# Kernel optimization log

Hardware: AMD Instinct MI355X
Metric: run time of the kernel (lower is better)

## Reference

```python
import jax, jax.numpy as jnp
import numpy as np

B = 8
C_IN = 3
IMG = 64
NF = 32
N_CALLS = 8
LAT = 512
KSIZES = [2 ** i + 1 for i in range(1, int(np.log2(IMG) - 1))]  # [3, 5, 9, 17]
N_SCALES = len(KSIZES)
C_FACTOR = 3 * N_SCALES          # identity + sobel-x + sobel-y per scale
GROUPS = C_FACTOR // 3           # 4
F = NF * C_FACTOR                # 384 expanded channels
CG = F // GROUPS                 # 96 channels per group
DK_TOT = 3 * GROUPS * CG * CG + 3 * F   # 111744 dynamic weights+biases
DK_HID = 2 * LAT                 # lat_factor = 2
OUT_CH = NF + NF + NF + 1        # 97 (multi_cut split sizes)
STATE = NF + NF * IMG + NF * IMG + IMG * IMG  # 8224


def _leaky(x):
    return jax.nn.leaky_relu(x, 0.2)


def _sobel_pair(k):
    c = jnp.linspace(-1.0, 1.0, k)
    gx = jnp.cos(0.5 * jnp.pi * c)[:, None] * jnp.sin(0.5 * jnp.pi * c)[None, :]
    return gx, gx.T


def sin_sobel(x):
    # fixed multi-scale depthwise sin-sobel filters, mode='split_out':
    # per scale concat [x, gx(x) all chans, gy(x) all chans]
    Bx, C, H, W = x.shape
    outs = []
    for k in KSIZES:
        gx, gy = _sobel_pair(k)
        w = jnp.broadcast_to(jnp.stack([gx, gy])[None], (C, 2, k, k)).reshape(C * 2, 1, k, k)
        p = (k - 1) // 2
        y = jax.lax.conv_general_dilated(x, w.astype(x.dtype), (1, 1), [(p, p), (p, p)],
                                         feature_group_count=C,
                                         dimension_numbers=('NCHW', 'OIHW', 'NCHW'))
        y = y.reshape(Bx, C, 2, H, W).transpose(0, 2, 1, 3, 4).reshape(Bx, 2 * C, H, W)
        outs.append(jnp.concatenate([x, y], axis=1))
    return jnp.concatenate(outs, axis=1)  # [B, 3*C*n_scales, H, W]


def instance_norm(x, eps=1e-5):
    m = x.mean(axis=(2, 3), keepdims=True)
    v = ((x - m) ** 2).mean(axis=(2, 3), keepdims=True)
    return (x - m) * jax.lax.rsqrt(v + eps)


def lin_res(x, Ws, bs, W0, b0, W1, b1):
    # LinearResidualBlock: shortcut + 0.1 * MLP
    return x @ Ws + bs + 0.1 * (_leaky(x @ W0 + b0) @ W1 + b1)


def conv1x1(x, w, b):
    return jnp.einsum('oi,bihw->bohw', w, x) + b[None, :, None, None]


def res_block(x, c0w, c0b, c1w, c1b, csw, csb):
    # ResidualBlock (1x1 convs): conv_s(x) + 0.1 * conv1(lrelu(conv0(lrelu(x))))
    dx = conv1x1(_leaky(x), c0w, c0b)
    dx = conv1x1(_leaky(dx), c1w, c1b)
    return conv1x1(x, csw, csb) + 0.1 * dx


def dyna_res_block(x, lat, Ws, bs, W0, b0, W1, b1):
    # DynaResidualBlock: per-sample grouped 1x1 conv weights generated from lat
    Bx, Fc, H, W = x.shape
    ks = lin_res(lat, Ws, bs, W0, b0, W1, b1)  # [B, DK_TOT]
    S = GROUPS * CG * CG
    k_in, k_mid, k_out, b_in, b_mid, b_out = jnp.split(
        ks, [S, 2 * S, 3 * S, 3 * S + Fc, 3 * S + 2 * Fc], axis=1)
    k_in = k_in.reshape(Bx, GROUPS, CG, CG)
    k_mid = k_mid.reshape(Bx, GROUPS, CG, CG)
    k_out = k_out.reshape(Bx, GROUPS, CG, CG)
    xg = x.reshape(Bx, GROUPS, CG, H, W)
    h = jnp.einsum('bgoi,bgihw->bgohw', k_in, xg) + b_in.reshape(Bx, GROUPS, CG, 1, 1)
    h = _leaky(h)
    h = jnp.einsum('bgoi,bgihw->bgohw', k_mid, h) + b_mid.reshape(Bx, GROUPS, CG, 1, 1)
    h = _leaky(h)
    h = jnp.einsum('bgoi,bgihw->bgohw', k_out, h) + b_out.reshape(Bx, GROUPS, CG, 1, 1)
    return x + h.reshape(Bx, Fc, H, W)  # identity shortcut (fin == fout)


def _forward(x, inj_lat, in_conv_w, in_conv_b, fl_Ws, fl_bs, fl_W0, fl_b0, fl_W1, fl_b1,
             dk_Ws, dk_bs, dk_W0, dk_b0, dk_W1, dk_b1,
             fc_c0w, fc_c0b, fc_c1w, fc_c1b, fc_csw, fc_csb,
             out_conv_w, out_conv_b, otl_w, otl_b):
    Bs = x.shape[0]
    out = conv1x1(x, in_conv_w, in_conv_b)
    out_embs = [out]
    lat = inj_lat
    for c in range(N_CALLS):
        lat = lat + 0.1 * lin_res(lat, fl_Ws[c], fl_bs[c], fl_W0[c], fl_b0[c], fl_W1[c], fl_b1[c])
        z = sin_sobel(out)
        z = instance_norm(z)
        z = z * jax.nn.sigmoid(dyna_res_block(z, lat, dk_Ws, dk_bs, dk_W0, dk_b0, dk_W1, dk_b1))
        z = res_block(z, fc_c0w, fc_c0b, fc_c1w, fc_c1b, fc_csw, fc_csb)
        out = out + 0.1 * z
        out_embs.append(out)
    # NOTE: source applies frac_conv(out) again here, but frac_conv expects
    # n_filter*c_factor (384) input channels while out has n_filter (32);
    # that line would raise in torch, so it is omitted (see notes).
    y = conv1x1(out, out_conv_w, out_conv_b)  # [B, 97, H, W]
    f, fh, fw, hw = jnp.split(y, [NF, 2 * NF, 3 * NF], axis=1)
    state = jnp.concatenate([
        f.mean(axis=(2, 3)),
        fh.mean(axis=3).reshape(Bs, -1),
        fw.mean(axis=2).reshape(Bs, -1),
        hw.reshape(Bs, -1),
    ], axis=1)  # [B, STATE]
    lat_out = state @ otl_w + otl_b
    return lat_out, jnp.stack(out_embs)


def setup_inputs():
    key = jax.random.key(0)
    ks = jax.random.split(key, 16)
    s = 0.02
    return {
        'x': jax.random.normal(ks[0], (B, C_IN, IMG, IMG), jnp.float32),
        'inj_lat': jax.random.normal(ks[1], (B, LAT), jnp.float32),
        'in_conv_w': jax.random.normal(ks[2], (NF, C_IN), jnp.float32) * s,
        'in_conv_b': jnp.zeros((NF,), jnp.float32),
        'fl_Ws': jax.random.normal(ks[3], (N_CALLS, LAT, LAT), jnp.float32) * s,
        'fl_bs': jnp.zeros((N_CALLS, LAT), jnp.float32),
        'fl_W0': jax.random.normal(ks[4], (N_CALLS, LAT, LAT), jnp.float32) * s,
        'fl_b0': jnp.zeros((N_CALLS, LAT), jnp.float32),
        'fl_W1': jax.random.normal(ks[5], (N_CALLS, LAT, LAT), jnp.float32) * s,
        'fl_b1': jnp.zeros((N_CALLS, LAT), jnp.float32),
        'dk_Ws': jax.random.normal(ks[6], (LAT, DK_TOT), jnp.float32) * s,
        'dk_bs': jnp.zeros((DK_TOT,), jnp.float32),
        'dk_W0': jax.random.normal(ks[7], (LAT, DK_HID), jnp.float32) * s,
        'dk_b0': jnp.zeros((DK_HID,), jnp.float32),
        'dk_W1': jax.random.normal(ks[8], (DK_HID, DK_TOT), jnp.float32) * s,
        'dk_b1': jnp.zeros((DK_TOT,), jnp.float32),
        'fc_c0w': jax.random.normal(ks[9], (F, F), jnp.float32) * s,
        'fc_c0b': jnp.zeros((F,), jnp.float32),
        'fc_c1w': jax.random.normal(ks[10], (NF, F), jnp.float32) * s,
        'fc_c1b': jnp.zeros((NF,), jnp.float32),
        'fc_csw': jax.random.normal(ks[11], (NF, F), jnp.float32) * s,
        'fc_csb': jnp.zeros((NF,), jnp.float32),
        'out_conv_w': jax.random.normal(ks[12], (OUT_CH, NF), jnp.float32) * s,
        'out_conv_b': jnp.zeros((OUT_CH,), jnp.float32),
        'otl_w': jax.random.normal(ks[13], (STATE, LAT), jnp.float32) * s,
        'otl_b': jnp.zeros((LAT,), jnp.float32),
    }


def reference(x, inj_lat, in_conv_w, in_conv_b, fl_Ws, fl_bs, fl_W0, fl_b0, fl_W1, fl_b1,
              dk_Ws, dk_bs, dk_W0, dk_b0, dk_W1, dk_b1,
              fc_c0w, fc_c0b, fc_c1w, fc_c1b, fc_csw, fc_csb,
              out_conv_w, out_conv_b, otl_w, otl_b):
    return _forward(x, inj_lat, in_conv_w, in_conv_b, fl_Ws, fl_bs, fl_W0, fl_b0, fl_W1, fl_b1,
                    dk_Ws, dk_bs, dk_W0, dk_b0, dk_W1, dk_b1,
                    fc_c0w, fc_c0b, fc_c1w, fc_c1b, fc_csw, fc_csb,
                    out_conv_w, out_conv_b, otl_w, otl_b)
```

## Files before the change

kernel.cpp:

```cpp
#include <hip/hip_runtime.h>

#define DEV __device__ __forceinline__

typedef __attribute__((ext_vector_type(4))) float  f32x4;
typedef __attribute__((ext_vector_type(8))) short  s16x8;
typedef __attribute__((ext_vector_type(4))) short  s16x4;

union FragU { s16x8 v; unsigned short h[8]; };
union U4    { s16x4 v; unsigned short h[4]; };

DEV float lrelu(float x){ return x > 0.f ? x : 0.2f*x; }
DEV unsigned short bfrne(float f){
    unsigned u = __builtin_bit_cast(unsigned, f);
    u += 0x7fffu + ((u>>16)&1u);
    return (unsigned short)(u>>16);
}
DEV float bf2f(unsigned short h){
    unsigned u = ((unsigned)h)<<16; return __builtin_bit_cast(float,u);
}
DEV f32x4 mfma16(s16x8 a, s16x8 b, f32x4 c){
    return __builtin_amdgcn_mfma_f32_16x16x32_bf16(a, b, c, 0, 0, 0);
}
DEV float wave_sum(float v){
    #pragma unroll
    for(int m=32;m>0;m>>=1) v += __shfl_xor(v, m, 64);
    return v;
}
DEV void blk_reduce2(float& a, float& b, float* sm){
    a = wave_sum(a); b = wave_sum(b);
    int wv = threadIdx.x>>6, ln = threadIdx.x&63;
    if(ln==0){ sm[wv*2]=a; sm[wv*2+1]=b; }
    __syncthreads();
    a = sm[0]+sm[2]+sm[4]+sm[6];
    b = sm[1]+sm[3]+sm[5]+sm[7];
    __syncthreads();
}

#define EMB   1048576
#define DKT   111744

__global__ __launch_bounds__(256) void k_init(
    float* state, float* latout, const float* otlb,
    float* lats, const float* inj,
    unsigned short* w016, const float* c0w,
    unsigned short* w116, const float* c1w,
    unsigned short* wcsh, unsigned short* wcsl, const float* csw,
    const float* x, const float* icw, const float* icb, float* out0)
{
    int i = blockIdx.x*256 + threadIdx.x;
    if(i < 65792){ state[i] = 0.f; return; }            i -= 65792;
    if(i < 4096){ latout[i] = otlb[i&511]; return; }    i -= 4096;
    if(i < 4096){ lats[i] = inj[i]; return; }           i -= 4096;
    if(i < 147456){
        int j = i&7, ln = (i>>3)&63, f2 = i>>9, mt = f2/12, kt = f2 - mt*12;
        w016[i] = bfrne(c0w[(mt*16 + (ln&15))*384 + kt*32 + (ln>>4)*8 + j]);
        return; }                                       i -= 147456;
    if(i < 12288){
        int j = i&7, ln = (i>>3)&63, f2 = i>>9, mt = f2/12, kt = f2 - mt*12;
        w116[i] = bfrne(c1w[(mt*16 + (ln&15))*384 + kt*32 + (ln>>4)*8 + j]);
        return; }                                       i -= 12288;
    if(i < 12288){
        int j = i&7, ln = (i>>3)&63, f2 = i>>9, mt = f2/12, kt = f2 - mt*12;
        wcsh[i] = bfrne(csw[(mt*16 + (ln&15))*384 + kt*32 + (ln>>4)*8 + j]);
        return; }                                       i -= 12288;
    if(i < 12288){
        int j = i&7, ln = (i>>3)&63, f2 = i>>9, mt = f2/12, kt = f2 - mt*12;
        float w = csw[(mt*16 + (ln&15))*384 + kt*32 + (ln>>4)*8 + j];
        unsigned short hh = bfrne(w);
        wcsl[i] = bfrne(w - bf2f(hh)); return; }        i -= 12288;
    if(i < 1048576){
        int p = i & 4095, o = (i>>12)&31, bb = i>>17;
        const float* xb = x + (size_t)bb*12288 + p;
        out0[i] = icb[o] + icw[o*3]*xb[0] + icw[o*3+1]*xb[4096] + icw[o*3+2]*xb[8192];
        return; }
}

__global__ __launch_bounds__(256) void k_latA(const float* __restrict__ lat,
    const float* __restrict__ Ws, const float* __restrict__ W0,
    float* __restrict__ ppS, float* __restrict__ ppH)
{
    __shared__ float ls[8][128];
    int t = threadIdx.x;
    int kb = blockIdx.y*128;
    for(int i=t;i<1024;i+=256) ls[i>>7][i&127] = lat[(i>>7)*512 + kb + (i&127)];
    __syncthreads();
    const float* W = blockIdx.z ? W0 : Ws;
    float* pp = blockIdx.z ? ppH : ppS;
    int j = blockIdx.x*128 + (t&127);
    int half = t>>7, klo = half*64;
    int p = blockIdx.y*2 + half;
    float acc[8] = {0,0,0,0,0,0,0,0};
    for(int kk=0;kk<64;kk++){
        float wv_ = W[(size_t)(kb+klo+kk)*512 + j];
        #pragma unroll
        for(int m=0;m<8;m++) acc[m] += ls[m][klo+kk]*wv_;
    }
    #pragma unroll
    for(int m=0;m<8;m++) pp[(size_t)(p*8+m)*512 + j] = acc[m];
}

__global__ __launch_bounds__(256) void k_latBC(const float* __restrict__ ppH,
    const float* __restrict__ flb0c,
    const float* __restrict__ W1, const float* __restrict__ b1c,
    const float* __restrict__ latc, const float* __restrict__ ppS,
    const float* __restrict__ flbsc, float* __restrict__ latn)
{
    __shared__ float lh[8][512];
    __shared__ float part[8][128];
    int t = threadIdx.x;
    for(int i=t;i<4096;i+=256){
        int m = i>>9, jj = i&511;
        float v = flb0c[jj];
        #pragma unroll
        for(int p=0;p<8;p++) v += ppH[(size_t)(p*8+m)*512 + jj];
        lh[m][jj] = lrelu(v);
    }
    __syncthreads();
    int j = blockIdx.x*128 + (t&127), half = t>>7;
    float acc[8] = {0,0,0,0,0,0,0,0};
    int k0 = half*256;
    for(int kk=k0;kk<k0+256;kk++){
        float w = W1[(size_t)kk*512 + j];
        #pragma unroll
        for(int m=0;m<8;m++) acc[m] += lh[m][kk]*w;
    }
    if(half==1){
        #pragma unroll
        for(int m=0;m<8;m++) part[m][t&127] = acc[m];
    }
    __syncthreads();
    if(half==0){
        #pragma unroll
        for(int m=0;m<8;m++){
            float sv = flbsc[j];
            #pragma unroll
            for(int p=0;p<8;p++) sv += ppS[(size_t)(p*8+m)*512 + j];
            float t1 = acc[m] + part[m][t&127] + b1c[j];
            latn[m*512+j] = latc[m*512+j] + 0.1f*sv + 0.01f*t1;
        }
    }
}

__global__ __launch_bounds__(256) void k_dkH(const float* __restrict__ latsAll,
    const float* __restrict__ W0, float* __restrict__ ppD)
{
    __shared__ float ls[64][128];
    int t = threadIdx.x;
    int kb = blockIdx.y*128;
    for(int i=t;i<8192;i+=256) ls[i>>7][i&127] = latsAll[(i>>7)*512 + kb + (i&127)];
    __syncthreads();
    int j = blockIdx.x*128 + (t&127);
    int ksub = t>>7;
    int p = blockIdx.y*2 + ksub;
    for(int mc=0;mc<4;mc++){
        float acc[16] = {0,0,0,0,0,0,0,0,0,0,0,0,0,0,0,0};
        for(int kk=0;kk<64;kk++){
            float wv_ = W0[(size_t)(kb + ksub*64 + kk)*1024 + j];
            #pragma unroll
            for(int mi=0;mi<16;mi++) acc[mi] += ls[mc*16+mi][ksub*64+kk]*wv_;
        }
        #pragma unroll
        for(int mi=0;mi<16;mi++) ppD[(size_t)(p*64 + mc*16+mi)*1024 + j] = acc[mi];
    }
}

__global__ __launch_bounds__(256) void k_dkAcvt(const float* __restrict__ latsAll,
    const float* __restrict__ ppD, const float* __restrict__ dkb0,
    unsigned short* __restrict__ Ahi, unsigned short* __restrict__ Alo)
{
    int i = blockIdx.x*256 + threadIdx.x;
    int m = i/1536, k = i - m*1536;
    float v;
    if(k < 512) v = latsAll[m*512 + k];
    else {
        int j = k - 512;
        float hv = dkb0[j];
        #pragma unroll
        for(int p=0;p<8;p++) hv += ppD[(size_t)(p*64+m)*1024 + j];
        v = 0.1f*lrelu(hv);
    }
    unsigned short hh = bfrne(v);
    Ahi[i] = hh; Alo[i] = bfrne(v - bf2f(hh));
}

__global__ __launch_bounds__(256) void k_dkMain(const unsigned short* __restrict__ Ahi,
    const unsigned short* __restrict__ Alo,
    const float* __restrict__ Wsb, const float* __restrict__ W1b,
    const float* __restrict__ bs, const float* __restrict__ b1,
    unsigned short* __restrict__ KSfh, unsigned short* __restrict__ KSfl,
    float* __restrict__ KSb32)
{
    __shared__ unsigned short Wh[64][138];
    __shared__ unsigned short Wl[64][138];
    __shared__ unsigned short Ah[64][72];
    __shared__ unsigned short Al[64][72];
    int t = threadIdx.x, wv = t>>6, lane = t&63, l15 = lane&15, lg = lane>>4, lkb = lg*8;
    int n0 = blockIdx.x*128;
    int sk = t>>5, sc = (t&31)*4;
    int am = t>>2, ac = (t&3)*16;

    f32x4 wreg[8];
    s16x8 ah0, ah1, al0, al1;
    {
        #pragma unroll
        for(int s=0;s<8;s++)
            wreg[s] = *(const f32x4*)(Wsb + (size_t)(sk + s*8)*DKT + n0 + sc);
        const unsigned short* Abh = Ahi + am*1536 + ac;
        const unsigned short* Abl = Alo + am*1536 + ac;
        ah0 = *(const s16x8*)(Abh);     ah1 = *(const s16x8*)(Abh + 8);
        al0 = *(const s16x8*)(Abl);     al1 = *(const s16x8*)(Abl + 8);
    }

    f32x4 acc[4][2];
    #pragma unroll
    for(int mt=0;mt<4;mt++){ acc[mt][0]=f32x4{0,0,0,0}; acc[mt][1]=f32x4{0,0,0,0}; }

    for(int kt=0;kt<24;kt++){
        #pragma unroll
        for(int s=0;s<8;s++){
            int k = sk + s*8;
            unsigned short hh[4], ll[4];
            #pragma unroll
            for(int e=0;e<4;e++){
                float w = wreg[s][e];
                hh[e] = bfrne(w); ll[e] = bfrne(w - bf2f(hh[e]));
            }
            *(unsigned*)(&Wh[k][sc])   = (unsigned)hh[0] | ((unsigned)hh[1]<<16);
            *(unsigned*)(&Wh[k][sc+2]) = (unsigned)hh[2] | ((unsigned)hh[3]<<16);
            *(unsigned*)(&Wl[k][sc])   = (unsigned)ll[0] | ((unsigned)ll[1]<<16);
            *(unsigned*)(&Wl[k][sc+2]) = (unsigned)ll[2] | ((unsigned)ll[3]<<16);
        }
        *(s16x8*)(&Ah[am][ac]) = ah0;  *(s16x8*)(&Ah[am][ac+8]) = ah1;
        *(s16x8*)(&Al[am][ac]) = al0;  *(s16x8*)(&Al[am][ac+8]) = al1;
        __syncthreads();
        if(kt < 23){
            int kn = kt+1;
            const float* Wb = (kn<8) ? (Wsb + (size_t)(kn*64)*DKT)
                                     : (W1b + (size_t)(kn*64-512)*DKT);
            #pragma unroll
            for(int s=0;s<8;s++)
                wreg[s] = *(const f32x4*)(Wb + (size_t)(sk + s*8)*DKT + n0 + sc);
            const unsigned short* Abh = Ahi + am*1536 + kn*64 + ac;
            const unsigned short* Abl = Alo + am*1536 + kn*64 + ac;
            ah0 = *(const s16x8*)(Abh);     ah1 = *(const s16x8*)(Abh + 8);
            al0 = *(const s16x8*)(Abl);     al1 = *(const s16x8*)(Abl + 8);
        }
        #pragma unroll
        for(int ks=0;ks<2;ks++){
            s16x8 afh[4], afl[4];
            #pragma unroll
            for(int mt=0;mt<4;mt++){
                afh[mt] = *(const s16x8*)(&Ah[mt*16+l15][ks*32+lkb]);
                afl[mt] = *(const s16x8*)(&Al[mt*16+l15][ks*32+lkb]);
            }
            #pragma unroll
            for(int nt=0;nt<2;nt++){
                int col = wv*32 + nt*16 + l15;
                FragU bh, bl;
                #pragma unroll
                for(int j=0;j<8;j++){
                    bh.h[j] = Wh[ks*32+lkb+j][col];
                    bl.h[j] = Wl[ks*32+lkb+j][col];
                }
                #pragma unroll
                for(int mt=0;mt<4;mt++){
                    acc[mt][nt] = mfma16(afh[mt], bh.v, acc[mt][nt]);
                    acc[mt][nt] = mfma16(afh[mt], bl.v, acc[mt][nt]);
                    acc[mt][nt] = mfma16(afl[mt], bh.v, acc[mt][nt]);
                }
            }
        }
        __syncthreads();
    }
    #pragma unroll
    for(int nt=0;nt<2;nt++){
        int n = n0 + wv*32 + nt*16 + l15;
        float bias = bs[n] + 0.1f*b1[n];
        bool isW = (n < 110592);
        size_t colpart = 0; int nb2 = 0;
        if(isW){
            int L = n / 36864, rem = n - L*36864;
            int g = rem / 9216; int rem2 = rem - g*9216;
            int oo = rem2 / 96; int kk = rem2 - oo*96;
            int lane2 = (((kk&31)>>3)<<4) + (oo&15);
            int f = (oo>>4)*3 + (kk>>5);
            colpart = ((((size_t)(g*3 + L))*18 + f)*64 + lane2)*8 + (kk&7);
        } else nb2 = n - 110592;
        #pragma unroll
        for(int mt=0;mt<4;mt++)
            #pragma unroll
            for(int q=0;q<4;q++){
                int row = mt*16 + lg*4 + q;
                float v = acc[mt][nt][q] + bias;
                unsigned short hh = bfrne(v);
                if(isW){
                    size_t dst = (size_t)row*110592 + colpart;
                    KSfh[dst] = hh;
                    KSfl[dst] = bfrne(v - bf2f(hh));
                } else {
                    KSb32[(size_t)row*1152 + nb2] = v;
                }
            }
    }
}

__global__ __launch_bounds__(256) void k_stat(const float* __restrict__ outPrev,
    float2* __restrict__ stats, float* __restrict__ gxy)
{
    __shared__ float img[4096], va[4096], vb[4096];
    __shared__ float ct[17], stp[17];
    __shared__ float red[8];
    int t = threadIdx.x, ch = blockIdx.x, b = blockIdx.y, s = blockIdx.z;
    const float* src = outPrev + ((size_t)b*32 + ch)*4096;
    float2* stc = stats + (b*32 + ch)*9;
    float* gb = gxy + ((size_t)(b*32 + ch)*8)*4096;
    for(int i=t;i<4096;i+=256) img[i] = src[i];
    __syncthreads();
    if(s == 0){
        float s0=0.f, s1=0.f;
        for(int i=t;i<4096;i+=256){ float v=img[i]; s0+=v; s1+=v*v; }
        blk_reduce2(s0, s1, red);
        float mu = s0*(1.f/4096.f);
        float var = s1*(1.f/4096.f) - mu*mu; var = var<0.f?0.f:var;
        if(t==0) stc[0] = make_float2(mu, rsqrtf(var + 1e-5f));
    }
    const int ksz[4] = {3,5,9,17};
    int k = ksz[s], p = (k-1)>>1;
    if(t < k){
        float cc = -1.f + 2.f*(float)t/(float)(k-1);
        ct[t]  = cosf(1.5707963267948966f*cc);
        stp[t] = sinf(1.5707963267948966f*cc);
    }
    __syncthreads();
    for(int i=t;i<4096;i+=256){
        int y = i>>6, x = i&63; float ac=0.f, as=0.f;
        for(int tt=0;tt<k;tt++){
            int yy = y+tt-p;
            if(yy>=0 && yy<64){ float f = img[yy*64+x]; ac += ct[tt]*f; as += stp[tt]*f; }
        }
        va[i]=ac; vb[i]=as;
    }
    __syncthreads();
    float gx0=0.f,gx1=0.f,gy0=0.f,gy1=0.f;
    float* g0 = gb + (size_t)(2*s)*4096;
    float* g1 = gb + (size_t)(2*s+1)*4096;
    for(int i=t;i<4096;i+=256){
        int y=i>>6, x=i&63; float gx=0.f, gy=0.f;
        for(int tt=0;tt<k;tt++){
            int xx = x+tt-p;
            if(xx>=0 && xx<64){ gx += stp[tt]*va[y*64+xx]; gy += ct[tt]*vb[y*64+xx]; }
        }
        g0[i] = gx; g1[i] = gy;
        gx0+=gx; gx1+=gx*gx; gy0+=gy; gy1+=gy*gy;
    }
    blk_reduce2(gx0, gx1, red);
    blk_reduce2(gy0, gy1, red);
    float mgx = gx0*(1.f/4096.f), vgx = gx1*(1.f/4096.f)-mgx*mgx; vgx=vgx<0.f?0.f:vgx;
    float mgy = gy0*(1.f/4096.f), vgy = gy1*(1.f/4096.f)-mgy*mgy; vgy=vgy<0.f?0.f:vgy;
    if(t==0){
        stc[1+2*s] = make_float2(mgx, rsqrtf(vgx+1e-5f));
        stc[2+2*s] = make_float2(mgy, rsqrtf(vgy+1e-5f));
    }
}

__global__ __launch_bounds__(512) void k_mega(const float* __restrict__ outPrev,
    const float2* __restrict__ stats, const float* __restrict__ gxy,
    const unsigned short* __restrict__ KSfh, const unsigned short* __restrict__ KSfl,
    const float* __restrict__ KSb32,
    const unsigned short* __restrict__ w016, const unsigned short* __restrict__ w116,
    const unsigned short* __restrict__ wcsh, const unsigned short* __restrict__ wcsl,
    const float* __restrict__ c0b, const float* __restrict__ c1b,
    const float* __restrict__ csb,
    float* __restrict__ outNext, int cCall)
{
    __shared__ __align__(16) unsigned short zth[12][4][64][8];
    __shared__ __align__(16) unsigned short ztl[12][4][64][8];
    __shared__ __align__(16) unsigned short lhf[25600];
    __shared__ float2 sst[288];
    int t = threadIdx.x, x = t&63, cq = t>>6;
    int y = blockIdx.x, b = blockIdx.y;
    const float* ob = outPrev + (size_t)b*131072;
    for(int i=t;i<288;i+=512) sst[i] = stats[b*288 + i];
    __syncthreads();
    int qh = cq>>1, qo = (cq&1)*4;
    {
        U4 idh, idl;
        #pragma unroll
        for(int i=0;i<4;i++){
            int ch = cq*4 + i;
            float v = ob[(size_t)ch*4096 + y*64 + x];
            float2 sr = sst[ch*9];
            float z = (v - sr.x)*sr.y;
            idh.h[i] = bfrne(z); idl.h[i] = bfrne(z - bf2f(idh.h[i]));
        }
        #pragma unroll
        for(int s=0;s<4;s++){
            *(s16x4*)(&zth[3*s][qh][x][qo]) = idh.v;
            *(s16x4*)(&ztl[3*s][qh][x][qo]) = idl.v;
        }
    }
    #pragma unroll 1
    for(int s=0;s<4;s++){
        U4 xh, xl, yh, yl;
        #pragma unroll
        for(int i=0;i<4;i++){
            int ch = cq*4 + i;
            const float* gsrc = gxy + ((size_t)(b*32 + ch)*8)*4096 + y*64 + x;
            float gx = gsrc[(size_t)(2*s)*4096];
            float gy = gsrc[(size_t)(2*s+1)*4096];
            float2 sx = sst[ch*9 + 1+2*s], sy = sst[ch*9 + 2+2*s];
            float zx = (gx - sx.x)*sx.y, zy = (gy - sy.x)*sy.y;
            xh.h[i] = bfrne(zx); xl.h[i] = bfrne(zx - bf2f(xh.h[i]));
            yh.h[i] = bfrne(zy); yl.h[i] = bfrne(zy - bf2f(yh.h[i]));
        }
        *(s16x4*)(&zth[3*s+1][qh][x][qo]) = xh.v;
        *(s16x4*)(&ztl[3*s+1][qh][x][qo]) = xl.v;
        *(s16x4*)(&zth[3*s+2][qh][x][qo]) = yh.v;
        *(s16x4*)(&ztl[3*s+2][qh][x][qo]) = yl.v;
    }
    __syncthreads();

    int lane = t&63, l15 = lane&15, lg = lane>>4, lkb = lg*8, w = cq;
    int pxslot = w&3, half = w>>2;
    int row = cCall*8 + b;
    int pxl = pxslot*16 + l15;
    unsigned short* lhh = &lhf[w*3200];
    unsigned short* lhl = &lhf[w*3200 + 1600];
    #pragma unroll 1
    for(int gi=0; gi<2; gi++){
        int g = half*2 + gi;
        const unsigned short* Kfh = KSfh + (size_t)((row*4 + g)*3)*9216;
        const unsigned short* Kfl = KSfl + (size_t)((row*4 + g)*3)*9216;
        const float* Bf = KSb32 + (size_t)row*1152 + g*96;

        f32x4 acc[6];
        #pragma unroll
        for(int mt=0;mt<6;mt++) acc[mt]=f32x4{0,0,0,0};
        #pragma unroll
        for(int kt=0;kt<3;kt++){
            s16x8 bh = *(const s16x8*)(&zth[g*3+kt][lg][pxl][0]);
            s16x8 bl = *(const s16x8*)(&ztl[g*3+kt][lg][pxl][0]);
            #pragma unroll
            for(int mt=0;mt<6;mt++){
                s16x8 ah = *(const s16x8*)(Kfh + ((mt*3+kt)*64 + lane)*8);
                s16x8 al = *(const s16x8*)(Kfl + ((mt*3+kt)*64 + lane)*8);
                acc[mt] = mfma16(ah, bh, acc[mt]);
                acc[mt] = mfma16(ah, bl, acc[mt]);
                acc[mt] = mfma16(al, bh, acc[mt]);
            }
        }
        #pragma unroll
        for(int mt=0;mt<6;mt++){
            int o0 = mt*16 + lg*4;
            f32x4 bb = *(const f32x4*)(Bf + o0);
            U4 hh, hl;
            #pragma unroll
            for(int q=0;q<4;q++){
                float v = lrelu(acc[mt][q] + bb[q]);
                hh.h[q] = bfrne(v); hl.h[q] = bfrne(v - bf2f(hh.h[q]));
            }
            *(s16x4*)(&lhh[l15*100 + o0]) = hh.v;
            *(s16x4*)(&lhl[l15*100 + o0]) = hl.v;
        }
        #pragma unroll
        for(int mt=0;mt<6;mt++) acc[mt]=f32x4{0,0,0,0};
        #pragma unroll
        for(int kt=0;kt<3;kt++){
            s16x8 bh = *(const s16x8*)(&lhh[l15*100 + kt*32+lkb]);
            s16x8 bl = *(const s16x8*)(&lhl[l15*100 + kt*32+lkb]);
            #pragma unroll
            for(int mt=0;mt<6;mt++){
                s16x8 ah = *(const s16x8*)(Kfh + 9216 + ((mt*3+kt)*64 + lane)*8);
                s16x8 al = *(const s16x8*)(Kfl + 9216 + ((mt*3+kt)*64 + lane)*8);
                acc[mt] = mfma16(ah, bh, acc[mt]);
                acc[mt] = mfma16(ah, bl, acc[mt]);
                acc[mt] = mfma16(al, bh, acc[mt]);
            }
        }
        #pragma unroll
        for(int mt=0;mt<6;mt++){
            int o0 = mt*16 + lg*4;
            f32x4 bb = *(const f32x4*)(Bf + 384 + o0);
            U4 hh, hl;
            #pragma unroll
            for(int q=0;q<4;q++){
                float v = lrelu(acc[mt][q] + bb[q]);
                hh.h[q] = bfrne(v); hl.h[q] = bfrne(v - bf2f(hh.h[q]));
            }
            *(s16x4*)(&lhh[l15*100 + o0]) = hh.v;
            *(s16x4*)(&lhl[l15*100 + o0]) = hl.v;
        }
        #pragma unroll
        for(int mt=0;mt<6;mt++) acc[mt]=f32x4{0,0,0,0};
        #pragma unroll
        for(int kt=0;kt<3;kt++){
            s16x8 bh = *(const s16x8*)(&lhh[l15*100 + kt*32+lkb]);
            s16x8 bl = *(const s16x8*)(&lhl[l15*100 + kt*32+lkb]);
            #pragma unroll
            for(int mt=0;mt<6;mt++){
                s16x8 ah = *(const s16x8*)(Kfh + 18432 + ((mt*3+kt)*64 + lane)*8);
                s16x8 al = *(const s16x8*)(Kfl + 18432 + ((mt*3+kt)*64 + lane)*8);
                acc[mt] = mfma16(ah, bh, acc[mt]);
                acc[mt] = mfma16(ah, bl, acc[mt]);
                acc[mt] = mfma16(al, bh, acc[mt]);
            }
        }
        #pragma unroll
        for(int mt=0;mt<6;mt++){
            int o0 = mt*16 + lg*4;
            f32x4 bb = *(const f32x4*)(Bf + 768 + o0);
            int part = g*3 + (o0>>5), cc = o0&31;
            int q8 = cc>>3, off = cc&7;
            U4 zvh, zvl;
            zvh.v = *(const s16x4*)(&zth[part][q8][pxl][off]);
            zvl.v = *(const s16x4*)(&ztl[part][q8][pxl][off]);
            U4 ozh;
            #pragma unroll
            for(int q=0;q<4;q++){
                float zf = bf2f(zvh.h[q]) + bf2f(zvl.h[q]);
                float d  = zf + acc[mt][q] + bb[q];
                float sg = 1.f/(1.f + __expf(-d));
                ozh.h[q] = bfrne(zf*sg);
            }
            *(s16x4*)(&zth[part][q8][pxl][off]) = ozh.v;
        }
    }
    __syncthreads();

    unsigned short* ldx = &lhf[pxslot*6272];
    f32x4 a1[12];
    #pragma unroll
    for(int lm=0;lm<12;lm++) a1[lm]=f32x4{0,0,0,0};
    #pragma unroll 1
    for(int kt=0;kt<12;kt++){
        FragU bzh, blz;
        bzh.v = *(const s16x8*)(&zth[kt][lg][pxl][0]);
        #pragma unroll
        for(int j=0;j<8;j++) blz.h[j] = bfrne(lrelu(bf2f(bzh.h[j])));
        #pragma unroll
        for(int lm=0;lm<12;lm++){
            int mt = half*12 + lm;
            s16x8 af = *(const s16x8*)(w016 + ((size_t)(mt*12+kt)<<9) + (lane<<3));
            a1[lm] = mfma16(af, blz.v, a1[lm]);
        }
    }
    #pragma unroll
    for(int lm=0;lm<12;lm++){
        int mt = half*12 + lm;
        int o0 = mt*16 + lg*4;
        f32x4 bb = *(const f32x4*)(c0b + o0);
        U4 hv;
        #pragma unroll
        for(int q=0;q<4;q++) hv.h[q] = bfrne(lrelu(a1[lm][q] + bb[q]));
        *(s16x4*)(&ldx[l15*392 + o0]) = hv.v;
    }
    __syncthreads();

    {
        int mt = half;
        f32x4 a2 = f32x4{0,0,0,0};
        f32x4 a3 = f32x4{0,0,0,0};
        #pragma unroll 1
        for(int kt=0;kt<12;kt++){
            s16x8 bh_ = *(const s16x8*)(&ldx[l15*392 + kt*32 + lkb]);
            s16x8 bzh = *(const s16x8*)(&zth[kt][lg][pxl][0]);
            s16x8 af1 = *(const s16x8*)(w116 + ((size_t)(mt*12+kt)<<9) + (lane<<3));
            a2 = mfma16(af1, bh_, a2);
            s16x8 wh = *(const s16x8*)(wcsh + ((size_t)(mt*12+kt)<<9) + (lane<<3));
            s16x8 wl = *(const s16x8*)(wcsl + ((size_t)(mt*12+kt)<<9) + (lane<<3));
            a3 = mfma16(wh, bzh, a3);
            a3 = mfma16(wl, bzh, a3);
        }
        int o0 = mt*16 + lg*4;
        #pragma unroll
        for(int q=0;q<4;q++){
            int o = o0+q;
            int px = y*64 + pxl;
            float dx2 = a2[q] + c1b[o];
            float r   = a3[q] + csb[o] + 0.1f*dx2;
            size_t oidx = (size_t)b*131072 + (size_t)o*4096 + px;
            outNext[oidx] = outPrev[oidx] + 0.1f*r;
        }
    }
}

__global__ __launch_bounds__(256) void k_head1(const float* __restrict__ outF,
    const float* __restrict__ wout, const float* __restrict__ bout, float* __restrict__ state)
{
    __shared__ float sw[97*32];
    __shared__ float sb_[97];
    __shared__ float fp[32];
    __shared__ float fwp[2048];
    int t = threadIdx.x, b = blockIdx.y, pxb = blockIdx.x*256;
    for(int i=t;i<97*32;i+=256) sw[i] = wout[i];
    if(t<97) sb_[t] = bout[t];
    if(t<32) fp[t] = 0.f;
    for(int i=t;i<2048;i+=256) fwp[i] = 0.f;
    __syncthreads();
    int px = pxb + t, lane = t&63, wv = t>>6;
    float xi[32];
    #pragma unroll
    for(int i=0;i<32;i++) xi[i] = outF[(size_t)b*131072 + (size_t)i*4096 + px];
    float* st = state + (size_t)b*8224;
    int row = (pxb>>6) + wv, x = lane;
    for(int o=0;o<97;o++){
        float acc = sb_[o];
        #pragma unroll
        for(int i=0;i<32;i++) acc += sw[o*32+i]*xi[i];
        if(o < 32){
            float s = wave_sum(acc);
            if(lane==0) atomicAdd(&fp[o], s);
        } else if(o < 64){
            float s = wave_sum(acc);
            if(lane==0) st[32 + (o-32)*64 + row] = s*(1.f/64.f);
        } else if(o < 96){
            atomicAdd(&fwp[(o-64)*64 + x], acc);
        } else {
            st[4128 + px] = acc;
        }
    }
    __syncthreads();
    if(t<32) atomicAdd(&st[t], fp[t]*(1.f/4096.f));
    for(int i=t;i<2048;i+=256) atomicAdd(&st[2080+i], fwp[i]*(1.f/64.f));
}

__global__ __launch_bounds__(256) void k_head2(const float* __restrict__ state,
    const float* __restrict__ otlw, float* __restrict__ latout)
{
    __shared__ float ss[8*514];
    int t = threadIdx.x, j = blockIdx.x*256 + t, s0 = blockIdx.y*514;
    for(int i=t;i<8*514;i+=256){ int bb=i/514, si=i-bb*514; ss[i] = state[(size_t)bb*8224 + s0 + si]; }
    __syncthreads();
    float acc[8] = {0,0,0,0,0,0,0,0};
    for(int si=0;si<514;si++){
        float wv_ = otlw[(size_t)(s0+si)*512 + j];
        #pragma unroll
        for(int b2=0;b2<8;b2++) acc[b2] += ss[b2*514+si]*wv_;
    }
    #pragma unroll
    for(int b2=0;b2<8;b2++) atomicAdd(latout + b2*512 + j, acc[b2]);
}

extern "C" void kernel_launch(void* const* d_in, const int* in_sizes, int n_in,
                              void* d_out, int out_size, void* d_ws, size_t ws_size,
                              hipStream_t stream)
{
    const float* x    = (const float*)d_in[0];
    const float* inj  = (const float*)d_in[1];
    const float* icw  = (const float*)d_in[2];
    const float* icb  = (const float*)d_in[3];
    const float* flWs = (const float*)d_in[4];
    const float* flbs = (const float*)d_in[5];
    const float* flW0 = (const float*)d_in[6];
    const float* flb0 = (const float*)d_in[7];
    const float* flW1 = (const float*)d_in[8];
    const float* flb1 = (const float*)d_in[9];
    const float* dkWs = (const float*)d_in[10];
    const float* dkbs = (const float*)d_in[11];
    const float* dkW0 = (const float*)d_in[12];
    const float* dkb0 = (const float*)d_in[13];
    const float* dkW1 = (const float*)d_in[14];
    const float* dkb1 = (const float*)d_in[15];
    const float* c0w  = (const float*)d_in[16];
    const float* c0b  = (const float*)d_in[17];
    const float* c1w  = (const float*)d_in[18];
    const float* c1b  = (const float*)d_in[19];
    const float* csw  = (const float*)d_in[20];
    const float* csb  = (const float*)d_in[21];
    const float* ocw  = (const float*)d_in[22];
    const float* ocb  = (const float*)d_in[23];
    const float* otlw = (const float*)d_in[24];
    const float* otlb = (const float*)d_in[25];
    float* out = (float*)d_out;

    char* wp = (char*)d_ws;
    auto carve = [&](size_t bytes)->void*{ void* p = wp; wp += (bytes + 255) & ~(size_t)255; return p; };
    float* lats  = (float*)carve(36864*4);
    float* ppS   = (float*)carve(32768*4);
    float* ppH   = (float*)carve(32768*4);
    float* ppD   = (float*)carve(524288*4);
    float* state = (float*)carve(65792*4);
    float2* stats = (float2*)carve(2304*8);
    float* gxy   = (float*)carve((size_t)8388608*4);
    unsigned short* Ahi   = (unsigned short*)carve((size_t)98304*2);
    unsigned short* Alo   = (unsigned short*)carve((size_t)98304*2);
    unsigned short* KSfh  = (unsigned short*)carve((size_t)7077888*2);
    unsigned short* KSfl  = (unsigned short*)carve((size_t)7077888*2);
    float*          KSb32 = (float*)carve((size_t)73728*4);
    unsigned short* w016  = (unsigned short*)carve((size_t)147456*2);
    unsigned short* w116  = (unsigned short*)carve((size_t)12288*2);
    unsigned short* wcsh  = (unsigned short*)carve((size_t)12288*2);
    unsigned short* wcsl  = (unsigned short*)carve((size_t)12288*2);

    k_init<<<5105,256,0,stream>>>(state, out, otlb, lats, inj,
                                  w016, c0w, w116, c1w, wcsh, wcsl, csw,
                                  x, icw, icb, out + 4096);

    for(int c=0;c<8;c++){
        const float* latc = lats + c*4096;
        k_latA<<<dim3(4,4,2),256,0,stream>>>(latc, flWs + (size_t)c*262144, flW0 + (size_t)c*262144,
                                             ppS, ppH);
        k_latBC<<<4,256,0,stream>>>(ppH, flb0 + (size_t)c*512,
                                    flW1 + (size_t)c*262144, flb1 + (size_t)c*512,
                                    latc, ppS, flbs + (size_t)c*512, lats + (c+1)*4096);
    }

    k_dkH<<<dim3(8,4),256,0,stream>>>(lats + 4096, dkW0, ppD);
    k_dkAcvt<<<384,256,0,stream>>>(lats + 4096, ppD, dkb0, Ahi, Alo);
    k_dkMain<<<873,256,0,stream>>>(Ahi, Alo, dkWs, dkW1, dkbs, dkb1, KSfh, KSfl, KSb32);

    for(int c=0;c<8;c++){
        const float* outPrev = out + 4096 + (size_t)c*EMB;
        float*       outNext = out + 4096 + (size_t)(c+1)*EMB;
        k_stat<<<dim3(32,8,4),256,0,stream>>>(outPrev, stats, gxy);
        k_mega<<<dim3(64,8),512,0,stream>>>(outPrev, stats, gxy, KSfh, KSfl, KSb32,
                                            w016, w116, wcsh, wcsl,
                                            c0b, c1b, csb, outNext, c);
    }

    k_head1<<<dim3(16,8),256,0,stream>>>(out + 4096 + (size_t)8*EMB, ocw, ocb, state);
    k_head2<<<dim3(2,16),256,0,stream>>>(state, otlw, out);
}
```

Measured before the change: 2.082 ms.

## Halve k_mega block to 4 waves, each wave processing two pixel tiles

Shrinks k_mega from 8 to 4 waves per block, and each wave now computes two 16-pixel tiles. That lets every weight fragment (Kfh/Kfl, w016, w116, wcs) loaded from global memory be reused for two MFMA tiles, halving weight-fetch traffic per pixel. In exchange each wave holds twice as many accumulators, which raises register pressure and may cut occupancy or cause spills. There are also fewer waves per block to hide latency.

```diff
diff --git a/kernel.cpp b/kernel.cpp
--- a/kernel.cpp
+++ b/kernel.cpp
@@ -363,7 +363,7 @@
     }
 }
 
-__global__ __launch_bounds__(512) void k_mega(const float* __restrict__ outPrev,
+__global__ __launch_bounds__(256) void k_mega(const float* __restrict__ outPrev,
     const float2* __restrict__ stats, const float* __restrict__ gxy,
     const unsigned short* __restrict__ KSfh, const unsigned short* __restrict__ KSfl,
     const float* __restrict__ KSb32,
@@ -380,14 +380,15 @@
     int t = threadIdx.x, x = t&63, cq = t>>6;
     int y = blockIdx.x, b = blockIdx.y;
     const float* ob = outPrev + (size_t)b*131072;
-    for(int i=t;i<288;i+=512) sst[i] = stats[b*288 + i];
-    __syncthreads();
-    int qh = cq>>1, qo = (cq&1)*4;
-    {
+    for(int i=t;i<288;i+=256) sst[i] = stats[b*288 + i];
+    __syncthreads();
+    int qh = cq;
+    #pragma unroll
+    for(int io=0;io<2;io++){
         U4 idh, idl;
         #pragma unroll
         for(int i=0;i<4;i++){
-            int ch = cq*4 + i;
+            int ch = cq*8 + io*4 + i;
             float v = ob[(size_t)ch*4096 + y*64 + x];
             float2 sr = sst[ch*9];
             float z = (v - sr.x)*sr.y;
@@ -395,37 +396,42 @@
         }
         #pragma unroll
         for(int s=0;s<4;s++){
-            *(s16x4*)(&zth[3*s][qh][x][qo]) = idh.v;
-            *(s16x4*)(&ztl[3*s][qh][x][qo]) = idl.v;
+            *(s16x4*)(&zth[3*s][qh][x][io*4]) = idh.v;
+            *(s16x4*)(&ztl[3*s][qh][x][io*4]) = idl.v;
         }
     }
     #pragma unroll 1
     for(int s=0;s<4;s++){
-        U4 xh, xl, yh, yl;
-        #pragma unroll
-        for(int i=0;i<4;i++){
-            int ch = cq*4 + i;
-            const float* gsrc = gxy + ((size_t)(b*32 + ch)*8)*4096 + y*64 + x;
-            float gx = gsrc[(size_t)(2*s)*4096];
-            float gy = gsrc[(size_t)(2*s+1)*4096];
-            float2 sx = sst[ch*9 + 1+2*s], sy = sst[ch*9 + 2+2*s];
-            float zx = (gx - sx.x)*sx.y, zy = (gy - sy.x)*sy.y;
-            xh.h[i] = bfrne(zx); xl.h[i] = bfrne(zx - bf2f(xh.h[i]));
-            yh.h[i] = bfrne(zy); yl.h[i] = bfrne(zy - bf2f(yh.h[i]));
-        }
-        *(s16x4*)(&zth[3*s+1][qh][x][qo]) = xh.v;
-        *(s16x4*)(&ztl[3*s+1][qh][x][qo]) = xl.v;
-        *(s16x4*)(&zth[3*s+2][qh][x][qo]) = yh.v;
-        *(s16x4*)(&ztl[3*s+2][qh][x][qo]) = yl.v;
+        #pragma unroll
+        for(int io=0;io<2;io++){
+            U4 xh, xl, yh, yl;
+            #pragma unroll
+            for(int i=0;i<4;i++){
+                int ch = cq*8 + io*4 + i;
+                const float* gsrc = gxy + ((size_t)(b*32 + ch)*8)*4096 + y*64 + x;
+                float gx = gsrc[(size_t)(2*s)*4096];
+                float gy = gsrc[(size_t)(2*s+1)*4096];
+                float2 sx = sst[ch*9 + 1+2*s], sy = sst[ch*9 + 2+2*s];
+                float zx = (gx - sx.x)*sx.y, zy = (gy - sy.x)*sy.y;
+                xh.h[i] = bfrne(zx); xl.h[i] = bfrne(zx - bf2f(xh.h[i]));
+                yh.h[i] = bfrne(zy); yl.h[i] = bfrne(zy - bf2f(yh.h[i]));
+            }
+            *(s16x4*)(&zth[3*s+1][qh][x][io*4]) = xh.v;
+            *(s16x4*)(&ztl[3*s+1][qh][x][io*4]) = xl.v;
+            *(s16x4*)(&zth[3*s+2][qh][x][io*4]) = yh.v;
+            *(s16x4*)(&ztl[3*s+2][qh][x][io*4]) = yl.v;
+        }
     }
     __syncthreads();
 
     int lane = t&63, l15 = lane&15, lg = lane>>4, lkb = lg*8, w = cq;
-    int pxslot = w&3, half = w>>2;
+    int half = w>>1, sp = w&1;
     int row = cCall*8 + b;
-    int pxl = pxslot*16 + l15;
-    unsigned short* lhh = &lhf[w*3200];
-    unsigned short* lhl = &lhf[w*3200 + 1600];
+    int pxl0 = sp*32 + l15, pxl1 = sp*32 + 16 + l15;
+    unsigned short* lh0h = &lhf[w*6400];
+    unsigned short* lh0l = &lhf[w*6400 + 1600];
+    unsigned short* lh1h = &lhf[w*6400 + 3200];
+    unsigned short* lh1l = &lhf[w*6400 + 4800];
     #pragma unroll 1
     for(int gi=0; gi<2; gi++){
         int g = half*2 + gi;
@@ -433,76 +439,99 @@
         const unsigned short* Kfl = KSfl + (size_t)((row*4 + g)*3)*9216;
         const float* Bf = KSb32 + (size_t)row*1152 + g*96;
 
-        f32x4 acc[6];
-        #pragma unroll
-        for(int mt=0;mt<6;mt++) acc[mt]=f32x4{0,0,0,0};
+        f32x4 a0[6], a1v[6];
+        #pragma unroll
+        for(int mt=0;mt<6;mt++){ a0[mt]=f32x4{0,0,0,0}; a1v[mt]=f32x4{0,0,0,0}; }
         #pragma unroll
         for(int kt=0;kt<3;kt++){
-            s16x8 bh = *(const s16x8*)(&zth[g*3+kt][lg][pxl][0]);
-            s16x8 bl = *(const s16x8*)(&ztl[g*3+kt][lg][pxl][0]);
+            s16x8 b0h = *(const s16x8*)(&zth[g*3+kt][lg][pxl0][0]);
+            s16x8 b0l = *(const s16x8*)(&ztl[g*3+kt][lg][pxl0][0]);
+            s16x8 b1h = *(const s16x8*)(&zth[g*3+kt][lg][pxl1][0]);
+            s16x8 b1l = *(const s16x8*)(&ztl[g*3+kt][lg][pxl1][0]);
             #pragma unroll
             for(int mt=0;mt<6;mt++){
                 s16x8 ah = *(const s16x8*)(Kfh + ((mt*3+kt)*64 + lane)*8);
                 s16x8 al = *(const s16x8*)(Kfl + ((mt*3+kt)*64 + lane)*8);
-                acc[mt] = mfma16(ah, bh, acc[mt]);
-                acc[mt] = mfma16(ah, bl, acc[mt]);
-                acc[mt] = mfma16(al, bh, acc[mt]);
+                a0[mt] = mfma16(ah, b0h, a0[mt]);
+                a0[mt] = mfma16(ah, b0l, a0[mt]);
+                a0[mt] = mfma16(al, b0h, a0[mt]);
+                a1v[mt] = mfma16(ah, b1h, a1v[mt]);
+                a1v[mt] = mfma16(ah, b1l, a1v[mt]);
+                a1v[mt] = mfma16(al, b1h, a1v[mt]);
             }
         }
         #pragma unroll
         for(int mt=0;mt<6;mt++){
             int o0 = mt*16 + lg*4;
             f32x4 bb = *(const f32x4*)(Bf + o0);
-            U4 hh, hl;
+            U4 h0h, h0l, h1h, h1l;
             #pragma unroll
             for(int q=0;q<4;q++){
-                float v = lrelu(acc[mt][q] + bb[q]);
-                hh.h[q] = bfrne(v); hl.h[q] = bfrne(v - bf2f(hh.h[q]));
-            }
-            *(s16x4*)(&lhh[l15*100 + o0]) = hh.v;
-            *(s16x4*)(&lhl[l15*100 + o0]) = hl.v;
-        }
-        #pragma unroll
-        for(int mt=0;mt<6;mt++) acc[mt]=f32x4{0,0,0,0};
+                float v0 = lrelu(a0[mt][q] + bb[q]);
+                h0h.h[q] = bfrne(v0); h0l.h[q] = bfrne(v0 - bf2f(h0h.h[q]));
+                float v1 = lrelu(a1v[mt][q] + bb[q]);
+                h1h.h[q] = bfrne(v1); h1l.h[q] = bfrne(v1 - bf2f(h1h.h[q]));
+            }
+            *(s16x4*)(&lh0h[l15*100 + o0]) = h0h.v;
+            *(s16x4*)(&lh0l[l15*100 + o0]) = h0l.v;
+            *(s16x4*)(&lh1h[l15*100 + o0]) = h1h.v;
+            *(s16x4*)(&lh1l[l15*100 + o0]) = h1l.v;
+        }
+        #pragma unroll
+        for(int mt=0;mt<6;mt++){ a0[mt]=f32x4{0,0,0,0}; a1v[mt]=f32x4{0,0,0,0}; }
         #pragma unroll
         for(int kt=0;kt<3;kt++){
-            s16x8 bh = *(const s16x8*)(&lhh[l15*100 + kt*32+lkb]);
-            s16x8 bl = *(const s16x8*)(&lhl[l15*100 + kt*32+lkb]);
+            s16x8 b0h = *(const s16x8*)(&lh0h[l15*100 + kt*32+lkb]);
+            s16x8 b0l = *(const s16x8*)(&lh0l[l15*100 + kt*32+lkb]);
+            s16x8 b1h = *(const s16x8*)(&lh1h[l15*100 + kt*32+lkb]);
+            s16x8 b1l = *(const s16x8*)(&lh1l[l15*100 + kt*32+lkb]);
             #pragma unroll
             for(int mt=0;mt<6;mt++){
                 s16x8 ah = *(const s16x8*)(Kfh + 9216 + ((mt*3+kt)*64 + lane)*8);
                 s16x8 al = *(const s16x8*)(Kfl + 9216 + ((mt*3+kt)*64 + lane)*8);
-                acc[mt] = mfma16(ah, bh, acc[mt]);
-                acc[mt] = mfma16(ah, bl, acc[mt]);
-                acc[mt] = mfma16(al, bh, acc[mt]);
+                a0[mt] = mfma16(ah, b0h, a0[mt]);
+                a0[mt] = mfma16(ah, b0l, a0[mt]);
+                a0[mt] = mfma16(al, b0h, a0[mt]);
+                a1v[mt] = mfma16(ah, b1h, a1v[mt]);
+                a1v[mt] = mfma16(ah, b1l, a1v[mt]);
+                a1v[mt] = mfma16(al, b1h, a1v[mt]);
             }
         }
         #pragma unroll
         for(int mt=0;mt<6;mt++){
             int o0 = mt*16 + lg*4;
             f32x4 bb = *(const f32x4*)(Bf + 384 + o0);
-            U4 hh, hl;
+            U4 h0h, h0l, h1h, h1l;
             #pragma unroll
             for(int q=0;q<4;q++){
-                float v = lrelu(acc[mt][q] + bb[q]);
-                hh.h[q] = bfrne(v); hl.h[q] = bfrne(v - bf2f(hh.h[q]));
-            }
-            *(s16x4*)(&lhh[l15*100 + o0]) = hh.v;
-            *(s16x4*)(&lhl[l15*100 + o0]) = hl.v;
-        }
-        #pragma unroll
-        for(int mt=0;mt<6;mt++) acc[mt]=f32x4{0,0,0,0};
+                float v0 = lrelu(a0[mt][q] + bb[q]);
+                h0h.h[q] = bfrne(v0); h0l.h[q] = bfrne(v0 - bf2f(h0h.h[q]));
+                float v1 = lrelu(a1v[mt][q] + bb[q]);
+                h1h.h[q] = bfrne(v1); h1l.h[q] = bfrne(v1 - bf2f(h1h.h[q]));
+            }
+            *(s16x4*)(&lh0h[l15*100 + o0]) = h0h.v;
+            *(s16x4*)(&lh0l[l15*100 + o0]) = h0l.v;
+            *(s16x4*)(&lh1h[l15*100 + o0]) = h1h.v;
+            *(s16x4*)(&lh1l[l15*100 + o0]) = h1l.v;
+        }
+        #pragma unroll
+        for(int mt=0;mt<6;mt++){ a0[mt]=f32x4{0,0,0,0}; a1v[mt]=f32x4{0,0,0,0}; }
         #pragma unroll
         for(int kt=0;kt<3;kt++){
-            s16x8 bh = *(const s16x8*)(&lhh[l15*100 + kt*32+lkb]);
-            s16x8 bl = *(const s16x8*)(&lhl[l15*100 + kt*32+lkb]);
+            s16x8 b0h = *(const s16x8*)(&lh0h[l15*100 + kt*32+lkb]);
+            s16x8 b0l = *(const s16x8*)(&lh0l[l15*100 + kt*32+lkb]);
+            s16x8 b1h = *(const s16x8*)(&lh1h[l15*100 + kt*32+lkb]);
+            s16x8 b1l = *(const s16x8*)(&lh1l[l15*100 + kt*32+lkb]);
             #pragma unroll
             for(int mt=0;mt<6;mt++){
                 s16x8 ah = *(const s16x8*)(Kfh + 18432 + ((mt*3+kt)*64 + lane)*8);
                 s16x8 al = *(const s16x8*)(Kfl + 18432 + ((mt*3+kt)*64 + lane)*8);
-                acc[mt] = mfma16(ah, bh, acc[mt]);
-                acc[mt] = mfma16(ah, bl, acc[mt]);
-                acc[mt] = mfma16(al, bh, acc[mt]);
+                a0[mt] = mfma16(ah, b0h, a0[mt]);
+                a0[mt] = mfma16(ah, b0l, a0[mt]);
+                a0[mt] = mfma16(al, b0h, a0[mt]);
+                a1v[mt] = mfma16(ah, b1h, a1v[mt]);
+                a1v[mt] = mfma16(ah, b1l, a1v[mt]);
+                a1v[mt] = mfma16(al, b1h, a1v[mt]);
             }
         }
         #pragma unroll
@@ -511,37 +540,47 @@
             f32x4 bb = *(const f32x4*)(Bf + 768 + o0);
             int part = g*3 + (o0>>5), cc = o0&31;
             int q8 = cc>>3, off = cc&7;
-            U4 zvh, zvl;
-            zvh.v = *(const s16x4*)(&zth[part][q8][pxl][off]);
-            zvl.v = *(const s16x4*)(&ztl[part][q8][pxl][off]);
-            U4 ozh;
+            U4 zvh0, zvl0, zvh1, zvl1, oz0, oz1;
+            zvh0.v = *(const s16x4*)(&zth[part][q8][pxl0][off]);
+            zvl0.v = *(const s16x4*)(&ztl[part][q8][pxl0][off]);
+            zvh1.v = *(const s16x4*)(&zth[part][q8][pxl1][off]);
+            zvl1.v = *(const s16x4*)(&ztl[part][q8][pxl1][off]);
             #pragma unroll
             for(int q=0;q<4;q++){
-                float zf = bf2f(zvh.h[q]) + bf2f(zvl.h[q]);
-                float d  = zf + acc[mt][q] + bb[q];
-                float sg = 1.f/(1.f + __expf(-d));
-                ozh.h[q] = bfrne(zf*sg);
-            }
-            *(s16x4*)(&zth[part][q8][pxl][off]) = ozh.v;
-        }
-    }
-    __syncthreads();
-
-    unsigned short* ldx = &lhf[pxslot*6272];
-    f32x4 a1[12];
-    #pragma unroll
-    for(int lm=0;lm<12;lm++) a1[lm]=f32x4{0,0,0,0};
+                float zf0 = bf2f(zvh0.h[q]) + bf2f(zvl0.h[q]);
+                float d0  = zf0 + a0[mt][q] + bb[q];
+                oz0.h[q] = bfrne(zf0 * (1.f/(1.f + __expf(-d0))));
+                float zf1 = bf2f(zvh1.h[q]) + bf2f(zvl1.h[q]);
+                float d1  = zf1 + a1v[mt][q] + bb[q];
+                oz1.h[q] = bfrne(zf1 * (1.f/(1.f + __expf(-d1))));
+            }
+            *(s16x4*)(&zth[part][q8][pxl0][off]) = oz0.v;
+            *(s16x4*)(&zth[part][q8][pxl1][off]) = oz1.v;
+        }
+    }
+    __syncthreads();
+
+    unsigned short* ldx0 = &lhf[(sp*2+0)*6272];
+    unsigned short* ldx1 = &lhf[(sp*2+1)*6272];
+    f32x4 a10[12], a11[12];
+    #pragma unroll
+    for(int lm=0;lm<12;lm++){ a10[lm]=f32x4{0,0,0,0}; a11[lm]=f32x4{0,0,0,0}; }
     #pragma unroll 1
     for(int kt=0;kt<12;kt++){
-        FragU bzh, blz;
-        bzh.v = *(const s16x8*)(&zth[kt][lg][pxl][0]);
-        #pragma unroll
-        for(int j=0;j<8;j++) blz.h[j] = bfrne(lrelu(bf2f(bzh.h[j])));
+        FragU bz0, bl0, bz1, bl1;
+        bz0.v = *(const s16x8*)(&zth[kt][lg][pxl0][0]);
+        bz1.v = *(const s16x8*)(&zth[kt][lg][pxl1][0]);
+        #pragma unroll
+        for(int j=0;j<8;j++){
+            bl0.h[j] = bfrne(lrelu(bf2f(bz0.h[j])));
+            bl1.h[j] = bfrne(lrelu(bf2f(bz1.h[j])));
+        }
         #pragma unroll
         for(int lm=0;lm<12;lm++){
             int mt = half*12 + lm;
             s16x8 af = *(const s16x8*)(w016 + ((size_t)(mt*12+kt)<<9) + (lane<<3));
-            a1[lm] = mfma16(af, blz.v, a1[lm]);
+            a10[lm] = mfma16(af, bl0.v, a10[lm]);
+            a11[lm] = mfma16(af, bl1.v, a11[lm]);
         }
     }
     #pragma unroll
@@ -549,37 +588,47 @@
         int mt = half*12 + lm;
         int o0 = mt*16 + lg*4;
         f32x4 bb = *(const f32x4*)(c0b + o0);
-        U4 hv;
-        #pragma unroll
-        for(int q=0;q<4;q++) hv.h[q] = bfrne(lrelu(a1[lm][q] + bb[q]));
-        *(s16x4*)(&ldx[l15*392 + o0]) = hv.v;
+        U4 h0, h1;
+        #pragma unroll
+        for(int q=0;q<4;q++){
+            h0.h[q] = bfrne(lrelu(a10[lm][q] + bb[q]));
+            h1.h[q] = bfrne(lrelu(a11[lm][q] + bb[q]));
+        }
+        *(s16x4*)(&ldx0[l15*392 + o0]) = h0.v;
+        *(s16x4*)(&ldx1[l15*392 + o0]) = h1.v;
     }
     __syncthreads();
 
     {
         int mt = half;
-        f32x4 a2 = f32x4{0,0,0,0};
-        f32x4 a3 = f32x4{0,0,0,0};
+        f32x4 a20 = f32x4{0,0,0,0}, a21 = f32x4{0,0,0,0};
+        f32x4 a30 = f32x4{0,0,0,0}, a31 = f32x4{0,0,0,0};
         #pragma unroll 1
         for(int kt=0;kt<12;kt++){
-            s16x8 bh_ = *(const s16x8*)(&ldx[l15*392 + kt*32 + lkb]);
-            s16x8 bzh = *(const s16x8*)(&zth[kt][lg][pxl][0]);
+            s16x8 bh0 = *(const s16x8*)(&ldx0[l15*392 + kt*32 + lkb]);
+            s16x8 bh1 = *(const s16x8*)(&ldx1[l15*392 + kt*32 + lkb]);
+            s16x8 bz0 = *(const s16x8*)(&zth[kt][lg][pxl0][0]);
+            s16x8 bz1 = *(const s16x8*)(&zth[kt][lg][pxl1][0]);
             s16x8 af1 = *(const s16x8*)(w116 + ((size_t)(mt*12+kt)<<9) + (lane<<3));
-            a2 = mfma16(af1, bh_, a2);
             s16x8 wh = *(const s16x8*)(wcsh + ((size_t)(mt*12+kt)<<9) + (lane<<3));
             s16x8 wl = *(const s16x8*)(wcsl + ((size_t)(mt*12+kt)<<9) + (lane<<3));
-            a3 = mfma16(wh, bzh, a3);
-            a3 = mfma16(wl, bzh, a3);
+            a20 = mfma16(af1, bh0, a20);
+            a21 = mfma16(af1, bh1, a21);
+            a30 = mfma16(wh, bz0, a30);
+            a30 = mfma16(wl, bz0, a30);
+            a31 = mfma16(wh, bz1, a31);
+            a31 = mfma16(wl, bz1, a31);
         }
         int o0 = mt*16 + lg*4;
         #pragma unroll
         for(int q=0;q<4;q++){
             int o = o0+q;
-            int px = y*64 + pxl;
-            float dx2 = a2[q] + c1b[o];
-            float r   = a3[q] + csb[o] + 0.1f*dx2;
-            size_t oidx = (size_t)b*131072 + (size_t)o*4096 + px;
-            outNext[oidx] = outPrev[oidx] + 0.1f*r;
+            float r0 = a30[q] + csb[o] + 0.1f*(a20[q] + c1b[o]);
+            float r1 = a31[q] + csb[o] + 0.1f*(a21[q] + c1b[o]);
+            size_t oi0 = (size_t)b*131072 + (size_t)o*4096 + y*64 + pxl0;
+            size_t oi1 = (size_t)b*131072 + (size_t)o*4096 + y*64 + pxl1;
+            outNext[oi0] = outPrev[oi0] + 0.1f*r0;
+            outNext[oi1] = outPrev[oi1] + 0.1f*r1;
         }
     }
 }
@@ -713,7 +762,7 @@
         const float* outPrev = out + 4096 + (size_t)c*EMB;
         float*       outNext = out + 4096 + (size_t)(c+1)*EMB;
         k_stat<<<dim3(32,8,4),256,0,stream>>>(outPrev, stats, gxy);
-        k_mega<<<dim3(64,8),512,0,stream>>>(outPrev, stats, gxy, KSfh, KSfl, KSb32,
+        k_mega<<<dim3(64,8),256,0,stream>>>(outPrev, stats, gxy, KSfh, KSfl, KSb32,
                                             w016, w116, wcsh, wcsl,
                                             c0b, c1b, csb, outNext, c);
     }
```

New measurement: 2.303 ms. 1.11x slower.
